# Kernel tuning notes

Measured on AMD Instinct MI355X. Metric: run time of the kernel, lower is better.

Reference implementation:

```python
import jax, jax.numpy as jnp
import numpy as np

EPS = 1e-6

def oneplus(x):
    return 1.0 + jnp.log1p(jnp.exp(x) + EPS)

def content_addr(mem, keys, strength):
    # mem [B,N,M], keys [B,R,M], strength [B,R] -> [B,R,N]
    mn = jnp.sqrt(jnp.sum(mem * mem, -1))    # [B,N]
    kn = jnp.sqrt(jnp.sum(keys * keys, -1))  # [B,R]
    sim = jnp.einsum('brm,bnm->brn', keys, mem) / (kn[..., None] * mn[:, None, :] + EPS)
    return jax.nn.softmax(strength[..., None] * sim, axis=-1)

def setup_inputs() -> dict:
    key = jax.random.key(0)
    ks = jax.random.split(key, 16)
    B, T, W, R, N, M = 16, 32, 128, 4, 512, 128
    def lin(k, fi, fo):
        k1, k2 = jax.random.split(k)
        s = 1.0 / np.sqrt(fi)
        return (jax.random.uniform(k1, (fi, fo), minval=-s, maxval=s),
                jax.random.uniform(k2, (fo,), minval=-s, maxval=s))
    Din = W + R * W  # controller input: cat(x_t, prev_reads)
    Wb, bb = lin(ks[0], Din + W, W)     # CfC backbone (1 layer, silu)
    Wff1, bff1 = lin(ks[1], W, W)
    Wff2, bff2 = lin(ks[2], W, W)
    Wta, bta = lin(ks[3], W, W)
    Wtb, btb = lin(ks[4], W, W)
    Wv, bv = lin(ks[5], W, W)
    Wr, br = lin(ks[6], W * R, W)
    Wxi, bxi = lin(ks[7], W, W * R + 3 * W + 5 * R + 3)
    X = jax.random.normal(ks[8], (B, T, W), dtype=jnp.float32)
    hs = jnp.zeros((B, W), dtype=jnp.float32)
    mem = jax.random.normal(ks[9], (B, N, M), dtype=jnp.float32) * 0.1
    reset_idxs = jax.random.randint(ks[10], (B, T), 0, 2, dtype=jnp.int32)
    return {'X': X, 'hs': hs, 'mem': mem, 'reset_idxs': reset_idxs,
            'Wb': Wb, 'bb': bb, 'Wff1': Wff1, 'bff1': bff1, 'Wff2': Wff2, 'bff2': bff2,
            'Wta': Wta, 'bta': bta, 'Wtb': Wtb, 'btb': btb,
            'Wv': Wv, 'bv': bv, 'Wr': Wr, 'br': br, 'Wxi': Wxi, 'bxi': bxi}

def dnc_forward(X, hs, mem, reset_idxs, Wb, bb, Wff1, bff1, Wff2, bff2,
                Wta, bta, Wtb, btb, Wv, bv, Wr, br, Wxi, bxi):
    B, T, W = X.shape
    N, M = mem.shape[1], mem.shape[2]
    R = (bxi.shape[0] - 3 * W - 3) // (W + 5)
    eye = jnp.eye(N, dtype=mem.dtype)

    def step(carry, inp):
        hs, memv, prev_reads, prev_rw, prev_ww, usage, prec, link = carry
        x_t, reset, t = inp
        r = reset.astype(x_t.dtype)
        memv = memv * (1 - r)[:, None, None]   # memory.reset_idx
        hs = hs * (1 - r)[:, None]
        # CfC controller cell
        z = jax.nn.silu(jnp.concatenate([x_t, prev_reads, hs], -1) @ Wb + bb)
        ff1 = z @ Wff1 + bff1
        ff2 = z @ Wff2 + bff2
        ti = jax.nn.sigmoid((z @ Wta + bta) * t + (z @ Wtb + btb))
        hs = ff1 * (1 - ti) + ti * ff2
        # interface vector split
        xi = hs @ Wxi + bxi
        p = 0
        read_keys = xi[:, :W * R].reshape(B, R, W); p = W * R
        write_key = xi[:, p:p + W]; p += W
        write_vec = xi[:, p:p + W]; p += W
        erase = jax.nn.sigmoid(xi[:, p:p + W]); p += W
        free_g = jax.nn.sigmoid(xi[:, p:p + R]); p += R
        read_str = oneplus(xi[:, p:p + R]); p += R
        read_modes = jax.nn.softmax(xi[:, p:p + 3 * R].reshape(B, R, 3), -1); p += 3 * R
        write_str = oneplus(xi[:, p:p + 1]); p += 1
        alloc_g = jax.nn.sigmoid(xi[:, p:p + 1]); p += 1
        write_g = jax.nn.sigmoid(xi[:, p:p + 1])
        # write weights
        wca = content_addr(memv, write_key[:, None, :], write_str)[:, 0]  # [B,N]
        retention = jnp.prod(1 - free_g[:, :, None] * prev_rw, axis=1)
        usage = (usage + prev_ww - usage * prev_ww) * retention
        si = jnp.argsort(usage, -1)
        cp = jnp.cumprod(jnp.take_along_axis(usage, si, -1), -1)
        alloc = (1 - usage) * jnp.take_along_axis(cp, si, -1)  # gather(1, sorted_idx), as in source
        ww = write_g * (alloc_g * alloc + (1 - alloc_g) * wca)  # [B,N]
        wc = ww[:, :, None]
        link = (1 - wc - jnp.swapaxes(wc, 1, 2)) * link + wc * prec[:, None, :]
        link = link * (1 - eye)
        prec = (1 - ww.sum(-1, keepdims=True)) * prec + ww
        memv = memv * (1 - wc * erase[:, None, :]) + wc * write_vec[:, None, :]
        # read
        rca = content_addr(memv, read_keys, read_str)              # [B,R,N]
        fw = jnp.einsum('brn,bnk->brk', prev_rw, link)
        bw = jnp.einsum('brn,bkn->brk', prev_rw, link)
        aux = jnp.stack([bw, rca, fw], 2)                          # [B,R,3,N]
        rw = (aux * read_modes[..., None]).sum(2)
        reads = jnp.einsum('brn,bnm->brm', rw, memv).reshape(B, R * M)
        y = hs @ Wv + bv + reads @ Wr + br
        # prev_reads is detached each step in the source
        carry = (hs, memv, jax.lax.stop_gradient(reads), rw, ww, usage, prec, link)
        return carry, (y, hs)

    dt = X.dtype
    init = (hs, mem,
            jnp.zeros((B, R * W), dt), jnp.zeros((B, R, N), dt), jnp.zeros((B, N), dt),
            jnp.zeros((B, N), dt), jnp.zeros((B, N), dt), jnp.zeros((B, N, N), dt))
    xs = (jnp.swapaxes(X, 0, 1), jnp.swapaxes(reset_idxs, 0, 1), jnp.arange(T, dtype=dt))
    _, (ys, hss) = jax.lax.scan(step, init, xs)
    return jnp.swapaxes(ys, 0, 1), jnp.swapaxes(hss, 0, 1)

def reference(X, hs, mem, reset_idxs, Wb, bb, Wff1, bff1, Wff2, bff2,
              Wta, bta, Wtb, btb, Wv, bv, Wr, br, Wxi, bxi):
    return dnc_forward(X, hs, mem, reset_idxs, Wb, bb, Wff1, bff1, Wff2, bff2,
                       Wta, bta, Wtb, btb, Wv, bv, Wr, br, Wxi, bxi)
```

## Files before the change

kernel.cpp:

```cpp
#include <hip/hip_runtime.h>
#include <math.h>

#define Bq 16
#define Tq 32
#define Wq 128
#define Rq 4
#define Nq 512
#define Mq 128
#define DINq 768
#define XIDq 919
#define BTWq (Bq*Tq*Wq)

#define TSTRIDE 31232
#define TF_FW    0
#define TF_BW    16384
#define TF_RCA   18432
#define TF_RW    20480
#define TF_PR    22528
#define TF_WC    26624
#define TF_WW    27136
#define TF_PREC  27648
#define TF_XI    28672
#define TF_CNT   29696

struct P {
  const float *X, *hs0, *mem0;
  const int *rst;
  const float *Wb,*bb,*Wff1,*bff1,*Wff2,*bff2,*Wta,*bta,*Wtb,*btb,*Wv,*bv,*Wr,*br,*Wxi,*bxi;
  float *out;
  float *rdh,*teams;
  float *WbT,*Wff1T,*Wff2T,*WtaT,*WtbT,*WvT,*WrT,*WxiT;
};

__device__ __forceinline__ float dot4(float4 a, float4 b){
  return a.x*b.x + a.y*b.y + a.z*b.z + a.w*b.w;
}
__device__ __forceinline__ float sigf(float x){ return 1.f/(1.f+expf(-x)); }
__device__ __forceinline__ float oneplusf(float x){ return 1.f + log1pf(expf(x) + 1e-6f); }

__device__ __forceinline__ void pst(float* p, float v){
  __hip_atomic_store(p, v, __ATOMIC_RELAXED, __HIP_MEMORY_SCOPE_AGENT);
}
__device__ __forceinline__ float pld(float* p){
  return __hip_atomic_load(p, __ATOMIC_RELAXED, __HIP_MEMORY_SCOPE_AGENT);
}
__device__ __forceinline__ void bump(unsigned* f){
  __syncthreads();
  if (threadIdx.x==0)
    __hip_atomic_fetch_add(f, 1u, __ATOMIC_RELAXED, __HIP_MEMORY_SCOPE_AGENT);
}
__device__ __forceinline__ void waitge(unsigned* f, unsigned v){
  if (threadIdx.x==0){
    while (__hip_atomic_fetch_add(f, 0u, __ATOMIC_RELAXED, __HIP_MEMORY_SCOPE_AGENT) < v)
      __builtin_amdgcn_s_sleep(1);
  }
  __syncthreads();
}

__device__ __forceinline__ float wave_sum64(float v){
  #pragma unroll
  for (int m=32;m>=1;m>>=1) v += __shfl_xor(v, m, 64);
  return v;
}
__device__ __forceinline__ float wave_max64(float v){
  #pragma unroll
  for (int m=32;m>=1;m>>=1) v = fmaxf(v, __shfl_xor(v, m, 64));
  return v;
}
__device__ __forceinline__ float blk_sum(float v, float* s8){
  int w = threadIdx.x>>6;
  v = wave_sum64(v);
  if ((threadIdx.x&63)==0) s8[w] = v;
  __syncthreads();
  float r = s8[0]+s8[1]+s8[2]+s8[3]+s8[4]+s8[5]+s8[6]+s8[7];
  __syncthreads();
  return r;
}
__device__ __forceinline__ float blk_max(float v, float* s8){
  int w = threadIdx.x>>6;
  v = wave_max64(v);
  if ((threadIdx.x&63)==0) s8[w] = v;
  __syncthreads();
  float r = s8[0];
  #pragma unroll
  for (int q=1;q<8;q++) r = fmaxf(r, s8[q]);
  __syncthreads();
  return r;
}

__global__ __launch_bounds__(256) void k_init(P p){
  int bid=blockIdx.x, tid=threadIdx.x;
  if (bid<8){ int idx=bid*256+tid, st=8*256;
    for (int k=idx;k<DINq*Wq;k+=st){ int j=k/DINq,i=k%DINq; p.WbT[k]=p.Wb[i*Wq+j]; }
  } else if (bid<10){ int idx=(bid-8)*256+tid, st=2*256;
    for (int k=idx;k<Wq*Wq;k+=st){ int j=k/Wq,i=k%Wq; p.Wff1T[k]=p.Wff1[i*Wq+j]; }
  } else if (bid<12){ int idx=(bid-10)*256+tid, st=2*256;
    for (int k=idx;k<Wq*Wq;k+=st){ int j=k/Wq,i=k%Wq; p.Wff2T[k]=p.Wff2[i*Wq+j]; }
  } else if (bid<14){ int idx=(bid-12)*256+tid, st=2*256;
    for (int k=idx;k<Wq*Wq;k+=st){ int j=k/Wq,i=k%Wq; p.WtaT[k]=p.Wta[i*Wq+j]; }
  } else if (bid<16){ int idx=(bid-14)*256+tid, st=2*256;
    for (int k=idx;k<Wq*Wq;k+=st){ int j=k/Wq,i=k%Wq; p.WtbT[k]=p.Wtb[i*Wq+j]; }
  } else if (bid<18){ int idx=(bid-16)*256+tid, st=2*256;
    for (int k=idx;k<Wq*Wq;k+=st){ int j=k/Wq,i=k%Wq; p.WvT[k]=p.Wv[i*Wq+j]; }
  } else if (bid<22){ int idx=(bid-18)*256+tid, st=4*256;
    for (int k=idx;k<Rq*Wq*Wq;k+=st){ int j=k/(Rq*Wq),i=k%(Rq*Wq); p.WrT[k]=p.Wr[i*Wq+j]; }
  } else if (bid<30){ int idx=(bid-22)*256+tid, st=8*256;
    for (int k=idx;k<XIDq*Wq;k+=st){ int f=k/Wq,i=k%Wq; p.WxiT[k]=p.Wxi[i*XIDq+f]; }
  } else if (bid<38){ int idx=(bid-30)*256+tid, st=8*256;
    for (int k=idx;k<16*TSTRIDE;k+=st) p.teams[k]=0.f;
  }
}

__global__ __launch_bounds__(512,2) void k_run(P p){
  const int tid=threadIdx.x, bid=blockIdx.x;
  const bool isA = (bid<16);
  const int team = isA ? bid : ((bid-16)>>3);
  const int g    = isA ? 0   : ((bid-16)&7);
  const int b=team;
  const int w=tid>>6, l=tid&63;
  float* T = p.teams + (size_t)team*TSTRIDE;
  unsigned* C = (unsigned*)(T+TF_CNT);
  unsigned* CNT_FW=C+0; unsigned* FLAG_RW=C+32; unsigned* CNT_RD=C+64;
  unsigned* FLAG_XI=C+96; unsigned* CNT_WC=C+128; unsigned* FLAG_WW=C+160;

  __shared__ __align__(16) float rwl[Rq*Nq];
  __shared__ __align__(16) float xil[XIDq+9];
  __shared__ __align__(16) float wwl[Nq];
  __shared__ __align__(16) float precl[Nq];
  __shared__ __align__(16) float usage[Nq];
  __shared__ __align__(16) float uarr[Nq];
  __shared__ __align__(16) float cpl[Nq];
  __shared__ __align__(16) int   sidx[Nq];
  __shared__ __align__(16) float wcas[Nq];
  __shared__ __align__(16) float inv[DINq];
  __shared__ __align__(16) float zl[Wq];
  __shared__ __align__(16) float hsl[Wq];
  __shared__ __align__(16) float acc4[4*Wq];
  __shared__ __align__(16) float scrA[Rq*Nq];
  __shared__ __align__(16) float scrB[Rq*Nq];
  __shared__ __align__(16) float scrC[Rq*Nq];
  __shared__ float s8[8];

  if (isA){
    for (int i=tid;i<Rq*Nq;i+=512) rwl[i]=0.f;
    usage[tid]=0.f; precl[tid]=0.f; wwl[tid]=0.f;
    if (tid<Wq) hsl[tid]=p.hs0[b*Wq+tid];
    __syncthreads();

    for (int t=0;t<=Tq;t++){
      if (t>0){
        waitge(CNT_FW, 8u*(unsigned)t);
        float* rcl=scrA; float* fwl=scrB; float* bwl=scrC;
        #pragma unroll
        for (int k=0;k<4;k++){
          int idx=tid+k*512;
          float f=0.f;
          #pragma unroll
          for (int gg=0;gg<8;gg++) f+=pld(T+TF_FW+gg*2048+idx);
          fwl[idx]=f;
          bwl[idx]=pld(T+TF_BW+idx);
          rcl[idx]=pld(T+TF_RCA+idx);
        }
        __syncthreads();
        #pragma unroll
        for (int r=0;r<Rq;r++){
          float v=rcl[r*Nq+tid];
          float mx=blk_max(v,s8);
          float e=expf(v-mx);
          float se=blk_sum(e,s8);
          rcl[r*Nq+tid]=e/se;
        }
        __syncthreads();
        #pragma unroll
        for (int k=0;k<4;k++){
          int idx=tid+k*512, r=idx>>9;
          float m0=xil[904+r*3],m1=xil[905+r*3],m2=xil[906+r*3];
          float mm=fmaxf(m0,fmaxf(m1,m2));
          float e0=expf(m0-mm),e1=expf(m1-mm),e2=expf(m2-mm);
          float es=e0+e1+e2;
          float rwv=(e0*bwl[idx]+e1*rcl[idx]+e2*fwl[idx])/es;
          rwl[idx]=rwv;
          pst(T+TF_RW+idx,rwv);
        }
      } else {
        #pragma unroll
        for (int k=0;k<4;k++){ int idx=tid+k*512; rwl[idx]=0.f; pst(T+TF_RW+idx,0.f); }
      }
      bump(FLAG_RW);
      waitge(CNT_RD, 8u*(unsigned)(t+1));
      if (t>0){
        float s=0.f;
        #pragma unroll
        for (int gg=0;gg<8;gg++) s+=pld(T+TF_PR+gg*512+tid);
        inv[Wq+tid]=s;
        p.rdh[((size_t)b*Tq+(t-1))*Nq+tid]=s;
      } else inv[Wq+tid]=0.f;
      if (t==Tq) break;
      __syncthreads();
      float keep=1.f-(float)p.rst[b*Tq+t];
      if (tid<Wq){ inv[tid]=p.X[((size_t)b*Tq+t)*Wq+tid]; inv[Wq+Nq+tid]=keep*hsl[tid]; }
      __syncthreads();
      { int j=tid>>2,q=tid&3;
        const float4* w4=(const float4*)(p.WbT+(size_t)j*DINq);
        const float4* i4=(const float4*)inv;
        float a=0.f;
        for (int c=q;c<192;c+=4) a+=dot4(w4[c],i4[c]);
        a+=__shfl_xor(a,1,4); a+=__shfl_xor(a,2,4);
        if (q==0){ a+=p.bb[j]; zl[j]=a*sigf(a); }
      }
      __syncthreads();
      { int which=tid>>7,j=tid&127;
        const float* Wg=(which==0)?p.Wff1T:(which==1)?p.Wff2T:(which==2)?p.WtaT:p.WtbT;
        const float4* w4=(const float4*)(Wg+(size_t)j*Wq);
        const float4* z4=(const float4*)zl;
        float a=0.f;
        #pragma unroll 8
        for (int c=0;c<32;c++) a+=dot4(w4[c],z4[c]);
        acc4[which*Wq+j]=a;
      }
      __syncthreads();
      if (tid<Wq){
        float a1=acc4[tid]+p.bff1[tid],a2=acc4[Wq+tid]+p.bff2[tid];
        float aa=acc4[2*Wq+tid]+p.bta[tid],ab=acc4[3*Wq+tid]+p.btb[tid];
        float ti=sigf(aa*(float)t+ab);
        float h=a1*(1.f-ti)+ti*a2;
        hsl[tid]=h;
        p.out[BTWq+((size_t)b*Tq+t)*Wq+tid]=h;
      }
      __syncthreads();
      { const float4* h4=(const float4*)hsl;
        { const float4* w4=(const float4*)(p.WxiT+(size_t)tid*Wq);
          float a=p.bxi[tid];
          #pragma unroll 8
          for (int c=0;c<32;c++) a+=dot4(w4[c],h4[c]);
          xil[tid]=a; pst(T+TF_XI+tid,a);
        }
        int f2=tid+512;
        if (f2<XIDq){
          const float4* w4=(const float4*)(p.WxiT+(size_t)f2*Wq);
          float a=p.bxi[f2];
          #pragma unroll 8
          for (int c=0;c<32;c++) a+=dot4(w4[c],h4[c]);
          xil[f2]=a; pst(T+TF_XI+f2,a);
        }
      }
      bump(FLAG_XI);
      int n=tid;
      float ret=1.f;
      #pragma unroll
      for (int r=0;r<Rq;r++) ret*=1.f-sigf(xil[896+r])*rwl[r*Nq+n];
      float uo=usage[n],pw=wwl[n];
      float u=(uo+pw-uo*pw)*ret;
      usage[n]=u; uarr[n]=u;
      __syncthreads();
      int rank=0;
      const float4* u4=(const float4*)uarr;
      #pragma unroll 8
      for (int jj=0;jj<128;jj++){
        float4 vv=u4[jj]; int j0=jj*4;
        rank+=(vv.x<u)||(vv.x==u&&(j0+0)<n);
        rank+=(vv.y<u)||(vv.y==u&&(j0+1)<n);
        rank+=(vv.z<u)||(vv.z==u&&(j0+2)<n);
        rank+=(vv.w<u)||(vv.w==u&&(j0+3)<n);
      }
      sidx[rank]=n;
      __syncthreads();
      int si=sidx[n];
      float sv=uarr[si];
      float x=sv;
      #pragma unroll
      for (int dd=1;dd<64;dd<<=1){ float pr=__shfl_up(x,dd,64); if (l>=dd) x*=pr; }
      if (l==63) s8[w]=x;
      __syncthreads();
      float woff=1.f;
      #pragma unroll
      for (int q=0;q<8;q++) if (q<w) woff*=s8[q];
      x*=woff;
      cpl[n]=x;
      waitge(CNT_WC, 8u*(unsigned)(t+1));
      { float v=pld(T+TF_WC+tid);
        float mx=blk_max(v,s8);
        float e=expf(v-mx);
        float se=blk_sum(e,s8);
        wcas[tid]=e/se;
      }
      __syncthreads();
      float alloc=(1.f-u)*cpl[si];
      float ag=sigf(xil[917]),wg=sigf(xil[918]);
      float wwv=wg*(ag*alloc+(1.f-ag)*wcas[n]);
      wwl[n]=wwv;
      pst(T+TF_WW+n,wwv);
      float wsum=blk_sum(wwv,s8);
      float pn=(1.f-wsum)*precl[n]+wwv;
      precl[n]=pn;
      pst(T+TF_PREC+(t&1)*Nq+n,pn);
      bump(FLAG_WW);
    }
  } else {
    const int rg=l>>3, cg=l&7;
    const int n_own=g*64+w*8+rg;
    const int c0=cg*16;
    float4 m4[4]; float nrm;
    { const float4* src=(const float4*)(p.mem0+((size_t)b*Nq+n_own)*Mq+c0);
      float s=0.f;
      #pragma unroll
      for (int i=0;i<4;i++){ m4[i]=src[i]; s+=dot4(m4[i],m4[i]); }
      s+=__shfl_xor(s,1,8); s+=__shfl_xor(s,2,8); s+=__shfl_xor(s,4,8);
      nrm=sqrtf(s);
    }
    float Lreg[8][8];
    #pragma unroll
    for (int rr=0;rr<8;rr++)
      #pragma unroll
      for (int q=0;q<8;q++) Lreg[rr][q]=0.f;

    for (int t=0;t<=Tq;t++){
      waitge(FLAG_RW, (unsigned)(t+1));
      for (int i=tid;i<Rq*Nq;i+=512) rwl[i]=pld(T+TF_RW+i);
      float* prl=wcas;
      prl[tid]=0.f;
      __syncthreads();
      #pragma unroll
      for (int r=0;r<Rq;r++){
        float rwn=rwl[r*Nq+n_own];
        #pragma unroll
        for (int i=0;i<4;i++){
          float ax=rwn*m4[i].x, ay=rwn*m4[i].y, az=rwn*m4[i].z, aw=rwn*m4[i].w;
          ax+=__shfl_xor(ax,8,64); ax+=__shfl_xor(ax,16,64); ax+=__shfl_xor(ax,32,64);
          ay+=__shfl_xor(ay,8,64); ay+=__shfl_xor(ay,16,64); ay+=__shfl_xor(ay,32,64);
          az+=__shfl_xor(az,8,64); az+=__shfl_xor(az,16,64); az+=__shfl_xor(az,32,64);
          aw+=__shfl_xor(aw,8,64); aw+=__shfl_xor(aw,16,64); aw+=__shfl_xor(aw,32,64);
          if (rg==0){
            atomicAdd(&prl[r*Wq+c0+i*4+0],ax);
            atomicAdd(&prl[r*Wq+c0+i*4+1],ay);
            atomicAdd(&prl[r*Wq+c0+i*4+2],az);
            atomicAdd(&prl[r*Wq+c0+i*4+3],aw);
          }
        }
      }
      __syncthreads();
      pst(T+TF_PR+g*512+tid, prl[tid]);
      bump(CNT_RD);
      if (t==Tq) break;
      waitge(FLAG_XI, (unsigned)(t+1));
      { xil[tid]=pld(T+TF_XI+tid);
        int f2=tid+512; if (f2<XIDq) xil[f2]=pld(T+TF_XI+f2); }
      __syncthreads();
      float keep=1.f-(float)p.rst[b*Tq+t];
      { float kk=(tid<Wq)? xil[512+tid]*xil[512+tid]:0.f;
        float kn=sqrtf(blk_sum(kk,s8));
        const float4* k4=(const float4*)(xil+512);
        float d=0.f;
        #pragma unroll
        for (int i=0;i<4;i++) d+=dot4(k4[cg*4+i],m4[i]);
        d+=__shfl_xor(d,1,8); d+=__shfl_xor(d,2,8); d+=__shfl_xor(d,4,8);
        float wstr=oneplusf(xil[916]);
        float sim=(keep*d)/(kn*(keep*nrm)+1e-6f);
        if (cg==0) pst(T+TF_WC+n_own, wstr*sim);
      }
      bump(CNT_WC);
      precl[tid]=pld(T+TF_PREC+((t&1)^1)*Nq+tid);
      waitge(FLAG_WW,(unsigned)(t+1));
      wwl[tid]=pld(T+TF_WW+tid);
      __syncthreads();
      { float* fwacc=scrA;
        int c0p=l*8;
        float ww8[8],pc8[8],pr8[Rq][8];
        *(float4*)&ww8[0]=*(const float4*)&wwl[c0p];   *(float4*)&ww8[4]=*(const float4*)&wwl[c0p+4];
        *(float4*)&pc8[0]=*(const float4*)&precl[c0p]; *(float4*)&pc8[4]=*(const float4*)&precl[c0p+4];
        #pragma unroll
        for (int r=0;r<Rq;r++){
          *(float4*)&pr8[r][0]=*(const float4*)&rwl[r*Nq+c0p];
          *(float4*)&pr8[r][4]=*(const float4*)&rwl[r*Nq+c0p+4];
        }
        float fa[Rq][8];
        #pragma unroll
        for (int r=0;r<Rq;r++)
          #pragma unroll
          for (int q=0;q<8;q++) fa[r][q]=0.f;
        #pragma unroll
        for (int rr=0;rr<8;rr++){
          int n2=g*64+w*8+rr;
          float wwn=wwl[n2];
          float prn[Rq];
          #pragma unroll
          for (int r=0;r<Rq;r++) prn[r]=rwl[r*Nq+n2];
          float bwp[Rq]={0.f,0.f,0.f,0.f};
          #pragma unroll
          for (int q=0;q<8;q++){
            float nv=(1.f-wwn-ww8[q])*Lreg[rr][q]+wwn*pc8[q];
            if (c0p+q==n2) nv=0.f;
            Lreg[rr][q]=nv;
            #pragma unroll
            for (int r=0;r<Rq;r++){ fa[r][q]+=prn[r]*nv; bwp[r]+=pr8[r][q]*nv; }
          }
          #pragma unroll
          for (int mm=1;mm<64;mm<<=1)
            #pragma unroll
            for (int r=0;r<Rq;r++) bwp[r]+=__shfl_xor(bwp[r],mm,64);
          if (l==0){
            #pragma unroll
            for (int r=0;r<Rq;r++) pst(T+TF_BW+r*Nq+n2, bwp[r]);
          }
        }
        for (int k=0;k<8;k++){
          if (w==k){
            #pragma unroll
            for (int r=0;r<Rq;r++)
              #pragma unroll
              for (int q=0;q<8;q++){
                if (k==0) fwacc[r*Nq+c0p+q]=fa[r][q];
                else      fwacc[r*Nq+c0p+q]+=fa[r][q];
              }
          }
          __syncthreads();
        }
        for (int i=tid;i<Rq*Nq;i+=512) pst(T+TF_FW+g*2048+i,fwacc[i]);
      }
      { float wwn=wwl[n_own];
        float s=0.f;
        #pragma unroll
        for (int i=0;i<4;i++){
          float e0=sigf(xil[768+c0+i*4+0]), e1=sigf(xil[768+c0+i*4+1]);
          float e2=sigf(xil[768+c0+i*4+2]), e3=sigf(xil[768+c0+i*4+3]);
          m4[i].x = m4[i].x*keep*(1.f-wwn*e0) + wwn*xil[640+c0+i*4+0];
          m4[i].y = m4[i].y*keep*(1.f-wwn*e1) + wwn*xil[640+c0+i*4+1];
          m4[i].z = m4[i].z*keep*(1.f-wwn*e2) + wwn*xil[640+c0+i*4+2];
          m4[i].w = m4[i].w*keep*(1.f-wwn*e3) + wwn*xil[640+c0+i*4+3];
          s+=dot4(m4[i],m4[i]);
        }
        s+=__shfl_xor(s,1,8); s+=__shfl_xor(s,2,8); s+=__shfl_xor(s,4,8);
        nrm=sqrtf(s);
        float kn4[Rq], rstr[Rq];
        #pragma unroll
        for (int r=0;r<Rq;r++){
          float kk=(tid<Wq)? xil[r*Wq+tid]*xil[r*Wq+tid]:0.f;
          kn4[r]=sqrtf(blk_sum(kk,s8));
          rstr[r]=oneplusf(xil[900+r]);
        }
        #pragma unroll
        for (int r=0;r<Rq;r++){
          const float4* kr=(const float4*)(xil+r*Wq);
          float d=0.f;
          #pragma unroll
          for (int i=0;i<4;i++) d+=dot4(kr[cg*4+i],m4[i]);
          d+=__shfl_xor(d,1,8); d+=__shfl_xor(d,2,8); d+=__shfl_xor(d,4,8);
          float v=rstr[r]*(d/(kn4[r]*nrm+1e-6f));
          if (cg==0) pst(T+TF_RCA+r*Nq+n_own, v);
        }
      }
      bump(CNT_FW);
    }
  }
}

__global__ __launch_bounds__(512) void k_y(P p){
  int j=blockIdx.x, tid=threadIdx.x;
  __shared__ __align__(16) float wv[Wq];
  __shared__ __align__(16) float wr[Rq*Wq];
  if (tid<Wq) wv[tid]=p.WvT[(size_t)j*Wq+tid];
  wr[tid]=p.WrT[(size_t)j*(Rq*Wq)+tid];
  __syncthreads();
  int b=tid>>5, t=tid&31;
  const float4* h4=(const float4*)(p.out+BTWq+((size_t)b*Tq+t)*Wq);
  const float4* r4=(const float4*)(p.rdh+((size_t)b*Tq+t)*Nq);
  const float4* wv4=(const float4*)wv;
  const float4* wr4=(const float4*)wr;
  float a=0.f;
  #pragma unroll 8
  for (int c=0;c<32;c++) a+=dot4(wv4[c],h4[c]);
  #pragma unroll 8
  for (int c=0;c<128;c++) a+=dot4(wr4[c],r4[c]);
  p.out[((size_t)b*Tq+t)*Wq+j]=a+p.bv[j]+p.br[j];
}

extern "C" void kernel_launch(void* const* d_in, const int* in_sizes, int n_in,
                              void* d_out, int out_size, void* d_ws, size_t ws_size,
                              hipStream_t stream){
  (void)in_sizes; (void)n_in; (void)out_size; (void)ws_size;
  P p;
  p.X    = (const float*)d_in[0];
  p.hs0  = (const float*)d_in[1];
  p.mem0 = (const float*)d_in[2];
  p.rst  = (const int*)d_in[3];
  p.Wb   = (const float*)d_in[4];  p.bb   = (const float*)d_in[5];
  p.Wff1 = (const float*)d_in[6];  p.bff1 = (const float*)d_in[7];
  p.Wff2 = (const float*)d_in[8];  p.bff2 = (const float*)d_in[9];
  p.Wta  = (const float*)d_in[10]; p.bta  = (const float*)d_in[11];
  p.Wtb  = (const float*)d_in[12]; p.btb  = (const float*)d_in[13];
  p.Wv   = (const float*)d_in[14]; p.bv   = (const float*)d_in[15];
  p.Wr   = (const float*)d_in[16]; p.br   = (const float*)d_in[17];
  p.Wxi  = (const float*)d_in[18]; p.bxi  = (const float*)d_in[19];
  p.out  = (float*)d_out;
  float* ws = (float*)d_ws;
  size_t o = 0;
  p.rdh   = ws + o; o += (size_t)Bq*Tq*Nq;
  p.teams = ws + o; o += (size_t)16*TSTRIDE;
  p.WbT   = ws + o; o += (size_t)DINq*Wq;
  p.Wff1T = ws + o; o += (size_t)Wq*Wq;
  p.Wff2T = ws + o; o += (size_t)Wq*Wq;
  p.WtaT  = ws + o; o += (size_t)Wq*Wq;
  p.WtbT  = ws + o; o += (size_t)Wq*Wq;
  p.WvT   = ws + o; o += (size_t)Wq*Wq;
  p.WrT   = ws + o; o += (size_t)Rq*Wq*Wq;
  p.WxiT  = ws + o; o += (size_t)XIDq*Wq;

  hipLaunchKernelGGL(k_init, dim3(38),  dim3(256), 0, stream, p);
  hipLaunchKernelGGL(k_run,  dim3(144), dim3(512), 0, stream, p);
  hipLaunchKernelGGL(k_y,    dim3(128), dim3(512), 0, stream, p);
}
```

Measured before the change: 2.567 ms.

## Compute read weights locally in worker blocks and split xi publication to shorten the critical path

Worker blocks now compute their own read weightings from partial softmax statistics (max and sum per group, published in a new TF_RMS region), along with locally kept backward and content values. This removes the wait on the controller block's FLAG_RW handoff before the memory read. The controller now overlaps the x and hidden parts of the backbone matvec with the wait for reads, and publishes the write key and scalar xi fields early under a new FLAG_WK flag so workers can start write content addressing sooner. These changes add redundant per-block softmax work and extra shared state, and they make the cross-block synchronisation more intricate.

```diff
diff --git a/kernel.cpp b/kernel.cpp
--- a/kernel.cpp
+++ b/kernel.cpp
@@ -11,7 +11,7 @@
 #define XIDq 919
 #define BTWq (Bq*Tq*Wq)
 
-#define TSTRIDE 31232
+#define TSTRIDE 30208
 #define TF_FW    0
 #define TF_BW    16384
 #define TF_RCA   18432
@@ -21,7 +21,8 @@
 #define TF_WW    27136
 #define TF_PREC  27648
 #define TF_XI    28672
-#define TF_CNT   29696
+#define TF_RMS   29696
+#define TF_CNT   29952
 
 struct P {
   const float *X, *hs0, *mem0;
@@ -51,7 +52,7 @@
 }
 __device__ __forceinline__ void waitge(unsigned* f, unsigned v){
   if (threadIdx.x==0){
-    while (__hip_atomic_fetch_add(f, 0u, __ATOMIC_RELAXED, __HIP_MEMORY_SCOPE_AGENT) < v)
+    while (__hip_atomic_load(f, __ATOMIC_RELAXED, __HIP_MEMORY_SCOPE_AGENT) < v)
       __builtin_amdgcn_s_sleep(1);
   }
   __syncthreads();
@@ -86,6 +87,12 @@
   for (int q=1;q<8;q++) r = fmaxf(r, s8[q]);
   __syncthreads();
   return r;
+}
+__device__ __forceinline__ float red_cg(float v){
+  v += __shfl_xor(v, 1, 8);
+  v += __shfl_xor(v, 2, 8);
+  v += __shfl_xor(v, 4, 8);
+  return v;
 }
 
 __global__ __launch_bounds__(256) void k_init(P p){
@@ -106,7 +113,7 @@
     for (int k=idx;k<Rq*Wq*Wq;k+=st){ int j=k/(Rq*Wq),i=k%(Rq*Wq); p.WrT[k]=p.Wr[i*Wq+j]; }
   } else if (bid<30){ int idx=(bid-22)*256+tid, st=8*256;
     for (int k=idx;k<XIDq*Wq;k+=st){ int f=k/Wq,i=k%Wq; p.WxiT[k]=p.Wxi[i*XIDq+f]; }
-  } else if (bid<38){ int idx=(bid-30)*256+tid, st=8*256;
+  } else if (bid<40){ int idx=(bid-30)*256+tid, st=10*256;
     for (int k=idx;k<16*TSTRIDE;k+=st) p.teams[k]=0.f;
   }
 }
@@ -120,8 +127,8 @@
   const int w=tid>>6, l=tid&63;
   float* T = p.teams + (size_t)team*TSTRIDE;
   unsigned* C = (unsigned*)(T+TF_CNT);
-  unsigned* CNT_FW=C+0; unsigned* FLAG_RW=C+32; unsigned* CNT_RD=C+64;
-  unsigned* FLAG_XI=C+96; unsigned* CNT_WC=C+128; unsigned* FLAG_WW=C+160;
+  unsigned* CNT_FW=C+0; unsigned* CNT_RD=C+32; unsigned* FLAG_WK=C+64;
+  unsigned* CNT_WC=C+96; unsigned* FLAG_WW=C+128;
 
   __shared__ __align__(16) float rwl[Rq*Nq];
   __shared__ __align__(16) float xil[XIDq+9];
@@ -139,16 +146,25 @@
   __shared__ __align__(16) float scrA[Rq*Nq];
   __shared__ __align__(16) float scrB[Rq*Nq];
   __shared__ __align__(16) float scrC[Rq*Nq];
+  __shared__ __align__(16) float bwown[Rq*64];
+  __shared__ __align__(16) float rcaown[Rq*64];
+  __shared__ __align__(16) float rwown[Rq*64];
+  __shared__ __align__(16) float rmst[64];
+  __shared__ __align__(16) float rmsM[4], rmsS[4];
+  __shared__ __align__(16) float modeE[16];
+  __shared__ __align__(16) float xisc[32];
   __shared__ float s8[8];
 
   if (isA){
-    for (int i=tid;i<Rq*Nq;i+=512) rwl[i]=0.f;
     usage[tid]=0.f; precl[tid]=0.f; wwl[tid]=0.f;
     if (tid<Wq) hsl[tid]=p.hs0[b*Wq+tid];
     __syncthreads();
 
     for (int t=0;t<=Tq;t++){
-      if (t>0){
+      if (t==0){
+        #pragma unroll
+        for (int k=0;k<4;k++){ int idx=tid+k*512; rwl[idx]=0.f; pst(T+TF_RW+idx,0.f); }
+      } else if (t<Tq){
         waitge(CNT_FW, 8u*(unsigned)t);
         float* rcl=scrA; float* fwl=scrB; float* bwl=scrC;
         #pragma unroll
@@ -182,11 +198,24 @@
           rwl[idx]=rwv;
           pst(T+TF_RW+idx,rwv);
         }
-      } else {
-        #pragma unroll
-        for (int k=0;k<4;k++){ int idx=tid+k*512; rwl[idx]=0.f; pst(T+TF_RW+idx,0.f); }
-      }
-      bump(FLAG_RW);
+        __syncthreads();
+      }
+      float keep=0.f;
+      if (t<Tq){
+        keep=1.f-(float)p.rst[b*Tq+t];
+        if (tid<Wq){ inv[tid]=p.X[((size_t)b*Tq+t)*Wq+tid]; inv[Wq+Nq+tid]=keep*hsl[tid]; }
+        __syncthreads();
+        int j=tid>>2,q=tid&3;
+        const float4* w4=(const float4*)(p.WbT+(size_t)j*DINq);
+        const float4* i4=(const float4*)inv;
+        float a=0.f;
+        #pragma unroll
+        for (int c=q;c<32;c+=4) a+=dot4(w4[c],i4[c]);
+        #pragma unroll
+        for (int c=160+q;c<192;c+=4) a+=dot4(w4[c],i4[c]);
+        a+=__shfl_xor(a,1,4); a+=__shfl_xor(a,2,4);
+        if (q==0) zl[j]=a+p.bb[j];
+      }
       waitge(CNT_RD, 8u*(unsigned)(t+1));
       if (t>0){
         float s=0.f;
@@ -197,16 +226,13 @@
       } else inv[Wq+tid]=0.f;
       if (t==Tq) break;
       __syncthreads();
-      float keep=1.f-(float)p.rst[b*Tq+t];
-      if (tid<Wq){ inv[tid]=p.X[((size_t)b*Tq+t)*Wq+tid]; inv[Wq+Nq+tid]=keep*hsl[tid]; }
-      __syncthreads();
       { int j=tid>>2,q=tid&3;
         const float4* w4=(const float4*)(p.WbT+(size_t)j*DINq);
         const float4* i4=(const float4*)inv;
         float a=0.f;
-        for (int c=q;c<192;c+=4) a+=dot4(w4[c],i4[c]);
+        for (int c=32+q;c<160;c+=4) a+=dot4(w4[c],i4[c]);
         a+=__shfl_xor(a,1,4); a+=__shfl_xor(a,2,4);
-        if (q==0){ a+=p.bb[j]; zl[j]=a*sigf(a); }
+        if (q==0){ float z=zl[j]+a; zl[j]=z*sigf(z); }
       }
       __syncthreads();
       { int which=tid>>7,j=tid&127;
@@ -229,22 +255,40 @@
       }
       __syncthreads();
       { const float4* h4=(const float4*)hsl;
+        { int o=tid>>2, q=tid&3; int f=512+o;
+          const float4* w4=(const float4*)(p.WxiT+(size_t)f*Wq);
+          float a=0.f;
+          #pragma unroll
+          for (int c=q;c<32;c+=4) a+=dot4(w4[c],h4[c]);
+          a+=__shfl_xor(a,1,4); a+=__shfl_xor(a,2,4);
+          if (q==0){ a+=p.bxi[f]; xil[f]=a; pst(T+TF_XI+f,a); }
+        }
+        if (tid<92){ int o=tid>>2, q=tid&3; int f=896+o;
+          const float4* w4=(const float4*)(p.WxiT+(size_t)f*Wq);
+          float a=0.f;
+          #pragma unroll
+          for (int c=q;c<32;c+=4) a+=dot4(w4[c],h4[c]);
+          a+=__shfl_xor(a,1,4); a+=__shfl_xor(a,2,4);
+          if (q==0){ a+=p.bxi[f]; xil[f]=a; pst(T+TF_XI+f,a); }
+        }
+      }
+      bump(FLAG_WK);
+      { const float4* h4=(const float4*)hsl;
         { const float4* w4=(const float4*)(p.WxiT+(size_t)tid*Wq);
           float a=p.bxi[tid];
           #pragma unroll 8
           for (int c=0;c<32;c++) a+=dot4(w4[c],h4[c]);
           xil[tid]=a; pst(T+TF_XI+tid,a);
         }
-        int f2=tid+512;
-        if (f2<XIDq){
-          const float4* w4=(const float4*)(p.WxiT+(size_t)f2*Wq);
-          float a=p.bxi[f2];
+        if (tid<256){ int f=640+tid;
+          const float4* w4=(const float4*)(p.WxiT+(size_t)f*Wq);
+          float a=p.bxi[f];
           #pragma unroll 8
           for (int c=0;c<32;c++) a+=dot4(w4[c],h4[c]);
-          xil[f2]=a; pst(T+TF_XI+f2,a);
-        }
-      }
-      bump(FLAG_XI);
+          xil[f]=a; pst(T+TF_XI+f,a);
+        }
+      }
+      __syncthreads();
       int n=tid;
       float ret=1.f;
       #pragma unroll
@@ -299,14 +343,14 @@
   } else {
     const int rg=l>>3, cg=l&7;
     const int n_own=g*64+w*8+rg;
+    const int row_own=w*8+rg;
     const int c0=cg*16;
     float4 m4[4]; float nrm;
     { const float4* src=(const float4*)(p.mem0+((size_t)b*Nq+n_own)*Mq+c0);
       float s=0.f;
       #pragma unroll
       for (int i=0;i<4;i++){ m4[i]=src[i]; s+=dot4(m4[i],m4[i]); }
-      s+=__shfl_xor(s,1,8); s+=__shfl_xor(s,2,8); s+=__shfl_xor(s,4,8);
-      nrm=sqrtf(s);
+      nrm=sqrtf(red_cg(s));
     }
     float Lreg[8][8];
     #pragma unroll
@@ -315,26 +359,51 @@
       for (int q=0;q<8;q++) Lreg[rr][q]=0.f;
 
     for (int t=0;t<=Tq;t++){
-      waitge(FLAG_RW, (unsigned)(t+1));
-      for (int i=tid;i<Rq*Nq;i+=512) rwl[i]=pld(T+TF_RW+i);
       float* prl=wcas;
       prl[tid]=0.f;
-      __syncthreads();
-      #pragma unroll
-      for (int r=0;r<Rq;r++){
-        float rwn=rwl[r*Nq+n_own];
-        #pragma unroll
-        for (int i=0;i<4;i++){
-          float ax=rwn*m4[i].x, ay=rwn*m4[i].y, az=rwn*m4[i].z, aw=rwn*m4[i].w;
-          ax+=__shfl_xor(ax,8,64); ax+=__shfl_xor(ax,16,64); ax+=__shfl_xor(ax,32,64);
-          ay+=__shfl_xor(ay,8,64); ay+=__shfl_xor(ay,16,64); ay+=__shfl_xor(ay,32,64);
-          az+=__shfl_xor(az,8,64); az+=__shfl_xor(az,16,64); az+=__shfl_xor(az,32,64);
-          aw+=__shfl_xor(aw,8,64); aw+=__shfl_xor(aw,16,64); aw+=__shfl_xor(aw,32,64);
-          if (rg==0){
-            atomicAdd(&prl[r*Wq+c0+i*4+0],ax);
-            atomicAdd(&prl[r*Wq+c0+i*4+1],ay);
-            atomicAdd(&prl[r*Wq+c0+i*4+2],az);
-            atomicAdd(&prl[r*Wq+c0+i*4+3],aw);
+      if (t>0){
+        waitge(CNT_FW, 8u*(unsigned)t);
+        if (tid<64){ rmst[tid]=pld(T+TF_RMS+tid); }
+        __syncthreads();
+        if (tid<4){
+          float M=-3.0e38f;
+          #pragma unroll
+          for (int gg=0;gg<8;gg++) M=fmaxf(M, rmst[gg*8+tid*2]);
+          float S=0.f;
+          #pragma unroll
+          for (int gg=0;gg<8;gg++) S+=expf(rmst[gg*8+tid*2]-M)*rmst[gg*8+tid*2+1];
+          rmsM[tid]=M; rmsS[tid]=S;
+        }
+        __syncthreads();
+        if (cg==0){
+          #pragma unroll
+          for (int r=0;r<Rq;r++){
+            float fwv=0.f;
+            #pragma unroll
+            for (int gg=0;gg<8;gg++) fwv+=pld(T+TF_FW+gg*2048+r*512+n_own);
+            float rca=expf(rcaown[r*64+row_own]-rmsM[r])/rmsS[r];
+            float rwv=(modeE[r*4+0]*bwown[r*64+row_own]+modeE[r*4+1]*rca
+                      +modeE[r*4+2]*fwv)/modeE[r*4+3];
+            rwown[r*64+row_own]=rwv;
+          }
+        }
+        __syncthreads();
+        #pragma unroll
+        for (int r=0;r<Rq;r++){
+          float rwn=rwown[r*64+row_own];
+          #pragma unroll
+          for (int i=0;i<4;i++){
+            float ax=rwn*m4[i].x, ay=rwn*m4[i].y, az=rwn*m4[i].z, aw=rwn*m4[i].w;
+            ax+=__shfl_xor(ax,8,64); ax+=__shfl_xor(ax,16,64); ax+=__shfl_xor(ax,32,64);
+            ay+=__shfl_xor(ay,8,64); ay+=__shfl_xor(ay,16,64); ay+=__shfl_xor(ay,32,64);
+            az+=__shfl_xor(az,8,64); az+=__shfl_xor(az,16,64); az+=__shfl_xor(az,32,64);
+            aw+=__shfl_xor(aw,8,64); aw+=__shfl_xor(aw,16,64); aw+=__shfl_xor(aw,32,64);
+            if (rg==0){
+              atomicAdd(&prl[r*Wq+c0+i*4+0],ax);
+              atomicAdd(&prl[r*Wq+c0+i*4+1],ay);
+              atomicAdd(&prl[r*Wq+c0+i*4+2],az);
+              atomicAdd(&prl[r*Wq+c0+i*4+3],aw);
+            }
           }
         }
       }
@@ -342,9 +411,16 @@
       pst(T+TF_PR+g*512+tid, prl[tid]);
       bump(CNT_RD);
       if (t==Tq) break;
-      waitge(FLAG_XI, (unsigned)(t+1));
-      { xil[tid]=pld(T+TF_XI+tid);
-        int f2=tid+512; if (f2<XIDq) xil[f2]=pld(T+TF_XI+f2); }
+      waitge(FLAG_WK, (unsigned)(t+1));
+      if (tid<Wq) xil[512+tid]=pld(T+TF_XI+512+tid);
+      if (tid<23) xisc[tid]=pld(T+TF_XI+896+tid);
+      __syncthreads();
+      if (tid<4){
+        float m0=xisc[8+tid*3],m1=xisc[9+tid*3],m2=xisc[10+tid*3];
+        float mm=fmaxf(m0,fmaxf(m1,m2));
+        float e0=expf(m0-mm),e1=expf(m1-mm),e2=expf(m2-mm);
+        modeE[tid*4+0]=e0; modeE[tid*4+1]=e1; modeE[tid*4+2]=e2; modeE[tid*4+3]=e0+e1+e2;
+      }
       __syncthreads();
       float keep=1.f-(float)p.rst[b*Tq+t];
       { float kk=(tid<Wq)? xil[512+tid]*xil[512+tid]:0.f;
@@ -353,8 +429,8 @@
         float d=0.f;
         #pragma unroll
         for (int i=0;i<4;i++) d+=dot4(k4[cg*4+i],m4[i]);
-        d+=__shfl_xor(d,1,8); d+=__shfl_xor(d,2,8); d+=__shfl_xor(d,4,8);
-        float wstr=oneplusf(xil[916]);
+        d=red_cg(d);
+        float wstr=oneplusf(xisc[20]);
         float sim=(keep*d)/(kn*(keep*nrm)+1e-6f);
         if (cg==0) pst(T+TF_WC+n_own, wstr*sim);
       }
@@ -362,6 +438,9 @@
       precl[tid]=pld(T+TF_PREC+((t&1)^1)*Nq+tid);
       waitge(FLAG_WW,(unsigned)(t+1));
       wwl[tid]=pld(T+TF_WW+tid);
+      for (int i=tid;i<Rq*Nq;i+=512) rwl[i]=pld(T+TF_RW+i);
+      xil[tid]=pld(T+TF_XI+tid);
+      if (tid<256) xil[640+tid]=pld(T+TF_XI+640+tid);
       __syncthreads();
       { float* fwacc=scrA;
         int c0p=l*8;
@@ -400,7 +479,7 @@
             for (int r=0;r<Rq;r++) bwp[r]+=__shfl_xor(bwp[r],mm,64);
           if (l==0){
             #pragma unroll
-            for (int r=0;r<Rq;r++) pst(T+TF_BW+r*Nq+n2, bwp[r]);
+            for (int r=0;r<Rq;r++){ pst(T+TF_BW+r*Nq+n2, bwp[r]); bwown[r*64+w*8+rr]=bwp[r]; }
           }
         }
         for (int k=0;k<8;k++){
@@ -423,20 +502,19 @@
         for (int i=0;i<4;i++){
           float e0=sigf(xil[768+c0+i*4+0]), e1=sigf(xil[768+c0+i*4+1]);
           float e2=sigf(xil[768+c0+i*4+2]), e3=sigf(xil[768+c0+i*4+3]);
-          m4[i].x = m4[i].x*keep*(1.f-wwn*e0) + wwn*xil[640+c0+i*4+0];
-          m4[i].y = m4[i].y*keep*(1.f-wwn*e1) + wwn*xil[640+c0+i*4+1];
-          m4[i].z = m4[i].z*keep*(1.f-wwn*e2) + wwn*xil[640+c0+i*4+2];
-          m4[i].w = m4[i].w*keep*(1.f-wwn*e3) + wwn*xil[640+c0+i*4+3];
+          m4[i].x=m4[i].x*keep*(1.f-wwn*e0)+wwn*xil[640+c0+i*4+0];
+          m4[i].y=m4[i].y*keep*(1.f-wwn*e1)+wwn*xil[640+c0+i*4+1];
+          m4[i].z=m4[i].z*keep*(1.f-wwn*e2)+wwn*xil[640+c0+i*4+2];
+          m4[i].w=m4[i].w*keep*(1.f-wwn*e3)+wwn*xil[640+c0+i*4+3];
           s+=dot4(m4[i],m4[i]);
         }
-        s+=__shfl_xor(s,1,8); s+=__shfl_xor(s,2,8); s+=__shfl_xor(s,4,8);
-        nrm=sqrtf(s);
+        nrm=sqrtf(red_cg(s));
         float kn4[Rq], rstr[Rq];
         #pragma unroll
         for (int r=0;r<Rq;r++){
           float kk=(tid<Wq)? xil[r*Wq+tid]*xil[r*Wq+tid]:0.f;
           kn4[r]=sqrtf(blk_sum(kk,s8));
-          rstr[r]=oneplusf(xil[900+r]);
+          rstr[r]=oneplusf(xisc[4+r]);
         }
         #pragma unroll
         for (int r=0;r<Rq;r++){
@@ -444,9 +522,18 @@
           float d=0.f;
           #pragma unroll
           for (int i=0;i<4;i++) d+=dot4(kr[cg*4+i],m4[i]);
-          d+=__shfl_xor(d,1,8); d+=__shfl_xor(d,2,8); d+=__shfl_xor(d,4,8);
+          d=red_cg(d);
           float v=rstr[r]*(d/(kn4[r]*nrm+1e-6f));
-          if (cg==0) pst(T+TF_RCA+r*Nq+n_own, v);
+          if (cg==0){ pst(T+TF_RCA+r*Nq+n_own, v); rcaown[r*64+row_own]=v; }
+        }
+        __syncthreads();
+        #pragma unroll
+        for (int r=0;r<Rq;r++){
+          float v=(tid<64)? rcaown[r*64+tid] : -3.0e38f;
+          float mx=blk_max(v,s8);
+          float e=(tid<64)? expf(v-mx):0.f;
+          float se=blk_sum(e,s8);
+          if (tid==0){ pst(T+TF_RMS+g*8+r*2, mx); pst(T+TF_RMS+g*8+r*2+1, se); }
         }
       }
       bump(CNT_FW);
@@ -505,7 +592,7 @@
   p.WrT   = ws + o; o += (size_t)Rq*Wq*Wq;
   p.WxiT  = ws + o; o += (size_t)XIDq*Wq;
 
-  hipLaunchKernelGGL(k_init, dim3(38),  dim3(256), 0, stream, p);
+  hipLaunchKernelGGL(k_init, dim3(40),  dim3(256), 0, stream, p);
   hipLaunchKernelGGL(k_run,  dim3(144), dim3(512), 0, stream, p);
   hipLaunchKernelGGL(k_y,    dim3(128), dim3(512), 0, stream, p);
 }
```

After: 2.949 ms. 1.15x slower.

## Shorten controller critical path: precompute backbone partials and publish write-head xi early

Applied to the files above, without the earlier changes.

Before waiting on the previous step's read results, the controller block now computes the part of the backbone matvec that does not depend on them (the x_t and hidden-state slices). Once the reads arrive, only the read-vector slice remains. It also computes the write-key and gate slices of the interface vector first, using 4 lanes per output, and signals FLAG_XI right after them. The memory blocks can then start write content addressing while the read keys and erase/write vectors are still being computed. The memory blocks load only the xi slices each phase needs, reading the rest later after FLAG_WW. The spin-wait now uses an atomic load instead of fetch_add. The added phases bring an extra sync, and correctness depends on the later xi slices being published before the FLAG_WW wait completes.

```diff
diff --git a/kernel.cpp b/kernel.cpp
--- a/kernel.cpp
+++ b/kernel.cpp
@@ -51,7 +51,7 @@
 }
 __device__ __forceinline__ void waitge(unsigned* f, unsigned v){
   if (threadIdx.x==0){
-    while (__hip_atomic_fetch_add(f, 0u, __ATOMIC_RELAXED, __HIP_MEMORY_SCOPE_AGENT) < v)
+    while (__hip_atomic_load(f, __ATOMIC_RELAXED, __HIP_MEMORY_SCOPE_AGENT) < v)
       __builtin_amdgcn_s_sleep(1);
   }
   __syncthreads();
@@ -86,6 +86,12 @@
   for (int q=1;q<8;q++) r = fmaxf(r, s8[q]);
   __syncthreads();
   return r;
+}
+__device__ __forceinline__ float red_cg(float v){
+  v += __shfl_xor(v, 1, 8);
+  v += __shfl_xor(v, 2, 8);
+  v += __shfl_xor(v, 4, 8);
+  return v;
 }
 
 __global__ __launch_bounds__(256) void k_init(P p){
@@ -187,6 +193,21 @@
         for (int k=0;k<4;k++){ int idx=tid+k*512; rwl[idx]=0.f; pst(T+TF_RW+idx,0.f); }
       }
       bump(FLAG_RW);
+      if (t<Tq){
+        float keep=1.f-(float)p.rst[b*Tq+t];
+        if (tid<Wq){ inv[tid]=p.X[((size_t)b*Tq+t)*Wq+tid]; inv[Wq+Nq+tid]=keep*hsl[tid]; }
+        __syncthreads();
+        int j=tid>>2,q=tid&3;
+        const float4* w4=(const float4*)(p.WbT+(size_t)j*DINq);
+        const float4* i4=(const float4*)inv;
+        float a=0.f;
+        #pragma unroll
+        for (int c=q;c<32;c+=4) a+=dot4(w4[c],i4[c]);
+        #pragma unroll
+        for (int c=160+q;c<192;c+=4) a+=dot4(w4[c],i4[c]);
+        a+=__shfl_xor(a,1,4); a+=__shfl_xor(a,2,4);
+        if (q==0) zl[j]=a+p.bb[j];
+      }
       waitge(CNT_RD, 8u*(unsigned)(t+1));
       if (t>0){
         float s=0.f;
@@ -197,16 +218,13 @@
       } else inv[Wq+tid]=0.f;
       if (t==Tq) break;
       __syncthreads();
-      float keep=1.f-(float)p.rst[b*Tq+t];
-      if (tid<Wq){ inv[tid]=p.X[((size_t)b*Tq+t)*Wq+tid]; inv[Wq+Nq+tid]=keep*hsl[tid]; }
-      __syncthreads();
       { int j=tid>>2,q=tid&3;
         const float4* w4=(const float4*)(p.WbT+(size_t)j*DINq);
         const float4* i4=(const float4*)inv;
         float a=0.f;
-        for (int c=q;c<192;c+=4) a+=dot4(w4[c],i4[c]);
+        for (int c=32+q;c<160;c+=4) a+=dot4(w4[c],i4[c]);
         a+=__shfl_xor(a,1,4); a+=__shfl_xor(a,2,4);
-        if (q==0){ a+=p.bb[j]; zl[j]=a*sigf(a); }
+        if (q==0){ float z=zl[j]+a; zl[j]=z*sigf(z); }
       }
       __syncthreads();
       { int which=tid>>7,j=tid&127;
@@ -229,22 +247,40 @@
       }
       __syncthreads();
       { const float4* h4=(const float4*)hsl;
+        { int o=tid>>2, q=tid&3; int f=512+o;
+          const float4* w4=(const float4*)(p.WxiT+(size_t)f*Wq);
+          float a=0.f;
+          #pragma unroll
+          for (int c=q;c<32;c+=4) a+=dot4(w4[c],h4[c]);
+          a+=__shfl_xor(a,1,4); a+=__shfl_xor(a,2,4);
+          if (q==0){ a+=p.bxi[f]; xil[f]=a; pst(T+TF_XI+f,a); }
+        }
+        if (tid<92){ int o=tid>>2, q=tid&3; int f=896+o;
+          const float4* w4=(const float4*)(p.WxiT+(size_t)f*Wq);
+          float a=0.f;
+          #pragma unroll
+          for (int c=q;c<32;c+=4) a+=dot4(w4[c],h4[c]);
+          a+=__shfl_xor(a,1,4); a+=__shfl_xor(a,2,4);
+          if (q==0){ a+=p.bxi[f]; xil[f]=a; pst(T+TF_XI+f,a); }
+        }
+      }
+      bump(FLAG_XI);
+      { const float4* h4=(const float4*)hsl;
         { const float4* w4=(const float4*)(p.WxiT+(size_t)tid*Wq);
           float a=p.bxi[tid];
           #pragma unroll 8
           for (int c=0;c<32;c++) a+=dot4(w4[c],h4[c]);
           xil[tid]=a; pst(T+TF_XI+tid,a);
         }
-        int f2=tid+512;
-        if (f2<XIDq){
-          const float4* w4=(const float4*)(p.WxiT+(size_t)f2*Wq);
-          float a=p.bxi[f2];
+        if (tid<256){ int f=640+tid;
+          const float4* w4=(const float4*)(p.WxiT+(size_t)f*Wq);
+          float a=p.bxi[f];
           #pragma unroll 8
           for (int c=0;c<32;c++) a+=dot4(w4[c],h4[c]);
-          xil[f2]=a; pst(T+TF_XI+f2,a);
-        }
-      }
-      bump(FLAG_XI);
+          xil[f]=a; pst(T+TF_XI+f,a);
+        }
+      }
+      __syncthreads();
       int n=tid;
       float ret=1.f;
       #pragma unroll
@@ -305,8 +341,7 @@
       float s=0.f;
       #pragma unroll
       for (int i=0;i<4;i++){ m4[i]=src[i]; s+=dot4(m4[i],m4[i]); }
-      s+=__shfl_xor(s,1,8); s+=__shfl_xor(s,2,8); s+=__shfl_xor(s,4,8);
-      nrm=sqrtf(s);
+      nrm=sqrtf(red_cg(s));
     }
     float Lreg[8][8];
     #pragma unroll
@@ -343,8 +378,8 @@
       bump(CNT_RD);
       if (t==Tq) break;
       waitge(FLAG_XI, (unsigned)(t+1));
-      { xil[tid]=pld(T+TF_XI+tid);
-        int f2=tid+512; if (f2<XIDq) xil[f2]=pld(T+TF_XI+f2); }
+      if (tid<Wq) xil[512+tid]=pld(T+TF_XI+512+tid);
+      if (tid<23) xil[896+tid]=pld(T+TF_XI+896+tid);
       __syncthreads();
       float keep=1.f-(float)p.rst[b*Tq+t];
       { float kk=(tid<Wq)? xil[512+tid]*xil[512+tid]:0.f;
@@ -353,7 +388,7 @@
         float d=0.f;
         #pragma unroll
         for (int i=0;i<4;i++) d+=dot4(k4[cg*4+i],m4[i]);
-        d+=__shfl_xor(d,1,8); d+=__shfl_xor(d,2,8); d+=__shfl_xor(d,4,8);
+        d=red_cg(d);
         float wstr=oneplusf(xil[916]);
         float sim=(keep*d)/(kn*(keep*nrm)+1e-6f);
         if (cg==0) pst(T+TF_WC+n_own, wstr*sim);
@@ -362,6 +397,8 @@
       precl[tid]=pld(T+TF_PREC+((t&1)^1)*Nq+tid);
       waitge(FLAG_WW,(unsigned)(t+1));
       wwl[tid]=pld(T+TF_WW+tid);
+      xil[tid]=pld(T+TF_XI+tid);
+      if (tid<256) xil[640+tid]=pld(T+TF_XI+640+tid);
       __syncthreads();
       { float* fwacc=scrA;
         int c0p=l*8;
@@ -423,14 +460,13 @@
         for (int i=0;i<4;i++){
           float e0=sigf(xil[768+c0+i*4+0]), e1=sigf(xil[768+c0+i*4+1]);
           float e2=sigf(xil[768+c0+i*4+2]), e3=sigf(xil[768+c0+i*4+3]);
-          m4[i].x = m4[i].x*keep*(1.f-wwn*e0) + wwn*xil[640+c0+i*4+0];
-          m4[i].y = m4[i].y*keep*(1.f-wwn*e1) + wwn*xil[640+c0+i*4+1];
-          m4[i].z = m4[i].z*keep*(1.f-wwn*e2) + wwn*xil[640+c0+i*4+2];
-          m4[i].w = m4[i].w*keep*(1.f-wwn*e3) + wwn*xil[640+c0+i*4+3];
+          m4[i].x=m4[i].x*keep*(1.f-wwn*e0)+wwn*xil[640+c0+i*4+0];
+          m4[i].y=m4[i].y*keep*(1.f-wwn*e1)+wwn*xil[640+c0+i*4+1];
+          m4[i].z=m4[i].z*keep*(1.f-wwn*e2)+wwn*xil[640+c0+i*4+2];
+          m4[i].w=m4[i].w*keep*(1.f-wwn*e3)+wwn*xil[640+c0+i*4+3];
           s+=dot4(m4[i],m4[i]);
         }
-        s+=__shfl_xor(s,1,8); s+=__shfl_xor(s,2,8); s+=__shfl_xor(s,4,8);
-        nrm=sqrtf(s);
+        nrm=sqrtf(red_cg(s));
         float kn4[Rq], rstr[Rq];
         #pragma unroll
         for (int r=0;r<Rq;r++){
@@ -444,7 +480,7 @@
           float d=0.f;
           #pragma unroll
           for (int i=0;i<4;i++) d+=dot4(kr[cg*4+i],m4[i]);
-          d+=__shfl_xor(d,1,8); d+=__shfl_xor(d,2,8); d+=__shfl_xor(d,4,8);
+          d=red_cg(d);
           float v=rstr[r]*(d/(kn4[r]*nrm+1e-6f));
           if (cg==0) pst(T+TF_RCA+r*Nq+n_own, v);
         }
```

Result: faster. 2.476 ms (-3.5%).
